# Kernel tuning notes

Measured on AMD Instinct MI355X. Metric: run time of the kernel, lower is better.

The kernel has to match this reference:

```python
import jax, jax.numpy as jnp
import numpy as np

B, T, X = 64, 8192, 32
LARGE_NUMBER = 1.0e6  # padding value for invalid (t' > t) entries in the original O(T^2) formulation


def setup_inputs() -> dict:
    key = jax.random.key(0)
    k1, k2 = jax.random.split(key)
    trace1 = jax.random.normal(k1, (B, T, X), dtype=jnp.float32)  # robustness trace of phi (time-reversed)
    trace2 = jax.random.normal(k2, (B, T, X), dtype=jnp.float32)  # robustness trace of psi (time-reversed)
    return {"trace1": trace1, "trace2": trace2}


def _until_trace(phi, psi):
    # phi, psi: [B, T, X] time-reversed traces (index 0 = final time step).
    # Original math (hard min/max, scale=-1, interval=None):
    #   out[j] = max_{j' <= j} min( psi[j'], min_{k in [j', j]} phi[k] )
    # which collapses exactly to the online recurrence:
    #   out[j] = min( phi[j], max( psi[j], out[j-1] ) ),  out[-1] = -LARGE_NUMBER
    # (min with a constant distributes over max). Single O(T) pass instead of O(T^2).
    phi_t = jnp.moveaxis(phi, 1, 0)  # [T, B, X]
    psi_t = jnp.moveaxis(psi, 1, 0)  # [T, B, X]
    init = jnp.full(phi_t.shape[1:], -LARGE_NUMBER, dtype=phi.dtype)  # [B, X]

    def step(carry, pp):
        p1, p2 = pp
        out = jnp.minimum(p1, jnp.maximum(p2, carry))
        return out, out

    _, outs = jax.lax.scan(step, init, (phi_t, psi_t))  # outs: [T, B, X]
    return jnp.moveaxis(outs, 0, 1)  # [B, T, X]


def reference(trace1, trace2):
    # Subformulas are Identity (pscale=1): robustness traces are the inputs themselves.
    return _until_trace(trace1, trace2)


if __name__ == "__main__":
    out = jax.jit(reference)(**setup_inputs())
    print(out.shape, out.dtype)
```

## Files before the change

kernel.cpp:

```cpp
#include <hip/hip_runtime.h>
#include <math.h>

constexpr int B_  = 64;
constexpr int T_  = 8192;
constexpr int X_  = 32;
constexpr int CH  = 256;
constexpr int TC  = T_ / CH;
constexpr int XG  = X_ / 4;
constexpr int CPL = CH / 64;
constexpr float NEG_LARGE = -1.0e6f;

typedef float vf4 __attribute__((ext_vector_type(4)));


__device__ __forceinline__ float4 clamp4(const float4 L, const float4 H, const float4 c) {
    return make_float4(fminf(H.x, fmaxf(L.x, c.x)),
                       fminf(H.y, fmaxf(L.y, c.y)),
                       fminf(H.z, fmaxf(L.z, c.z)),
                       fminf(H.w, fmaxf(L.w, c.w)));
}

__device__ __forceinline__ void compose_pair(const float4 p, const float4 q,
                                             float4& L, float4& H) {
    float l;
    l = fminf(p.x, q.x); L.x = fminf(p.x, fmaxf(l, L.x)); H.x = fminf(p.x, fmaxf(l, H.x));
    l = fminf(p.y, q.y); L.y = fminf(p.y, fmaxf(l, L.y)); H.y = fminf(p.y, fmaxf(l, H.y));
    l = fminf(p.z, q.z); L.z = fminf(p.z, fmaxf(l, L.z)); H.z = fminf(p.z, fmaxf(l, H.z));
    l = fminf(p.w, q.w); L.w = fminf(p.w, fmaxf(l, L.w)); H.w = fminf(p.w, fmaxf(l, H.w));
}

__device__ __forceinline__ void apply_step(const float4 p, const float4 q, float4& c) {
    c.x = fminf(p.x, fmaxf(q.x, c.x));
    c.y = fminf(p.y, fmaxf(q.y, c.y));
    c.z = fminf(p.z, fmaxf(q.z, c.z));
    c.w = fminf(p.w, fmaxf(q.w, c.w));
}

__device__ __forceinline__ float4 shfl_up4(const float4 v, int d) {
    return make_float4(__shfl_up(v.x, d, 64), __shfl_up(v.y, d, 64),
                       __shfl_up(v.z, d, 64), __shfl_up(v.w, d, 64));
}

__global__ __launch_bounds__(256) void until_pass1(
        const float4* __restrict__ phi, const float4* __restrict__ psi,
        float4* __restrict__ Lw, float4* __restrict__ Hw) {
    const int tid = blockIdx.x * 256 + threadIdx.x;
    const int xg  = tid & (XG - 1);
    const int bj  = tid / XG;
    const int j   = bj & (CH - 1);
    const int b   = bj / CH;
    const size_t base = ((size_t)b * T_ + (size_t)j * TC) * XG + xg;

    float4 L = make_float4(-INFINITY, -INFINITY, -INFINITY, -INFINITY);
    float4 H = make_float4( INFINITY,  INFINITY,  INFINITY,  INFINITY);
    #pragma unroll 4
    for (int t = 0; t < TC; ++t) {
        const float4 p = phi[base + (size_t)t * XG];
        const float4 q = psi[base + (size_t)t * XG];
        compose_pair(p, q, L, H);
    }
    Lw[(size_t)bj * XG + xg] = L;
    Hw[(size_t)bj * XG + xg] = H;
}

__global__ __launch_bounds__(256) void until_pass2(
        const float4* __restrict__ Lw, const float4* __restrict__ Hw,
        float4* __restrict__ Cw) {
    const int tid  = blockIdx.x * 256 + threadIdx.x;
    const int lane = tid & 63;
    const int w    = tid >> 6;
    const int xg   = w & (XG - 1);
    const int b    = w / XG;

    float4 cL[CPL], cH[CPL];
    float4 L = make_float4(-INFINITY, -INFINITY, -INFINITY, -INFINITY);
    float4 H = make_float4( INFINITY,  INFINITY,  INFINITY,  INFINITY);
    #pragma unroll
    for (int k = 0; k < CPL; ++k) {
        const int j = lane * CPL + k;
        const size_t idx = ((size_t)b * CH + j) * XG + xg;
        cL[k] = Lw[idx];
        cH[k] = Hw[idx];
        L = clamp4(cL[k], cH[k], L);
        H = clamp4(cL[k], cH[k], H);
    }

    #pragma unroll
    for (int d = 1; d < 64; d <<= 1) {
        const float4 Lp = shfl_up4(L, d);
        const float4 Hp = shfl_up4(H, d);
        if (lane >= d) {
            const float4 nL = clamp4(L, H, Lp);
            const float4 nH = clamp4(L, H, Hp);
            L = nL; H = nH;
        }
    }

    const float4 Lex = shfl_up4(L, 1);
    const float4 Hex = shfl_up4(H, 1);
    const float4 c0 = make_float4(NEG_LARGE, NEG_LARGE, NEG_LARGE, NEG_LARGE);
    float4 c = (lane == 0) ? c0 : clamp4(Lex, Hex, c0);

    #pragma unroll
    for (int k = 0; k < CPL; ++k) {
        const int j = lane * CPL + k;
        const size_t idx = ((size_t)b * CH + j) * XG + xg;
        Cw[idx] = c;
        c = clamp4(cL[k], cH[k], c);
    }
}

__global__ __launch_bounds__(256) void until_pass3(
        const float4* __restrict__ phi, const float4* __restrict__ psi,
        const float4* __restrict__ Cw, float4* __restrict__ out) {
    const int tid = blockIdx.x * 256 + threadIdx.x;
    const int xg  = tid & (XG - 1);
    const int bj  = tid / XG;
    const int j   = bj & (CH - 1);
    const int b   = bj / CH;
    const size_t base = ((size_t)b * T_ + (size_t)j * TC) * XG + xg;

    float4 c = Cw[(size_t)bj * XG + xg];
    #pragma unroll 4
    for (int t = 0; t < TC; ++t) {
        const float4 p = phi[base + (size_t)t * XG];
        const float4 q = psi[base + (size_t)t * XG];
        apply_step(p, q, c);
        vf4 cv; cv.x = c.x; cv.y = c.y; cv.z = c.z; cv.w = c.w;
        __builtin_nontemporal_store(cv, reinterpret_cast<vf4*>(&out[base + (size_t)t * XG]));
    }
}

extern "C" void kernel_launch(void* const* d_in, const int* in_sizes, int n_in,
                              void* d_out, int out_size, void* d_ws, size_t ws_size,
                              hipStream_t stream) {
    const float4* phi = (const float4*)d_in[0];
    const float4* psi = (const float4*)d_in[1];
    float4* out = (float4*)d_out;

    const size_t nsum = (size_t)B_ * CH * XG;
    float4* Lw = (float4*)d_ws;
    float4* Hw = Lw + nsum;
    float4* Cw = Hw + nsum;

    const int threads_main = B_ * CH * XG;
    until_pass1<<<threads_main / 256, 256, 0, stream>>>(phi, psi, Lw, Hw);
    until_pass2<<<(B_ * XG * 64) / 256, 256, 0, stream>>>(Lw, Hw, Cw);
    until_pass3<<<threads_main / 256, 256, 0, stream>>>(phi, psi, Cw, out);
}
```

Before: 208.3 us.

## Double chunk count, batch loads for memory-level parallelism, reuse workspace in scan

The chunk count CH becomes a template parameter, and the launcher picks 512 chunks when the workspace is large enough, doubling the thread count in passes 1 and 3. Those passes now issue eight phi loads and eight psi loads before computing, which increases outstanding memory requests per thread. Pass 2 no longer holds chunk summaries in registers: it reloads them and writes the carry-in values back over Lw in place, dropping the separate Cw buffer. The trade-offs are a longer in-warp scan (8 chunks per lane) and a redundant reload in pass 2.

```diff
diff --git a/kernel.cpp b/kernel.cpp
--- a/kernel.cpp
+++ b/kernel.cpp
@@ -4,10 +4,7 @@
 constexpr int B_  = 64;
 constexpr int T_  = 8192;
 constexpr int X_  = 32;
-constexpr int CH  = 256;
-constexpr int TC  = T_ / CH;
 constexpr int XG  = X_ / 4;
-constexpr int CPL = CH / 64;
 constexpr float NEG_LARGE = -1.0e6f;
 
 typedef float vf4 __attribute__((ext_vector_type(4)));
@@ -41,9 +38,11 @@
                        __shfl_up(v.z, d, 64), __shfl_up(v.w, d, 64));
 }
 
+template<int CH>
 __global__ __launch_bounds__(256) void until_pass1(
         const float4* __restrict__ phi, const float4* __restrict__ psi,
         float4* __restrict__ Lw, float4* __restrict__ Hw) {
+    constexpr int TC = T_ / CH;
     const int tid = blockIdx.x * 256 + threadIdx.x;
     const int xg  = tid & (XG - 1);
     const int bj  = tid / XG;
@@ -53,36 +52,40 @@
 
     float4 L = make_float4(-INFINITY, -INFINITY, -INFINITY, -INFINITY);
     float4 H = make_float4( INFINITY,  INFINITY,  INFINITY,  INFINITY);
-    #pragma unroll 4
-    for (int t = 0; t < TC; ++t) {
-        const float4 p = phi[base + (size_t)t * XG];
-        const float4 q = psi[base + (size_t)t * XG];
-        compose_pair(p, q, L, H);
+    constexpr int BATCH = 8;
+    for (int t0 = 0; t0 < TC; t0 += BATCH) {
+        float4 p[BATCH], q[BATCH];
+        #pragma unroll
+        for (int k = 0; k < BATCH; ++k) p[k] = phi[base + (size_t)(t0 + k) * XG];
+        #pragma unroll
+        for (int k = 0; k < BATCH; ++k) q[k] = psi[base + (size_t)(t0 + k) * XG];
+        #pragma unroll
+        for (int k = 0; k < BATCH; ++k) compose_pair(p[k], q[k], L, H);
     }
     Lw[(size_t)bj * XG + xg] = L;
     Hw[(size_t)bj * XG + xg] = H;
 }
 
+template<int CH>
 __global__ __launch_bounds__(256) void until_pass2(
-        const float4* __restrict__ Lw, const float4* __restrict__ Hw,
-        float4* __restrict__ Cw) {
+        float4* __restrict__ Lw, const float4* __restrict__ Hw) {
+    constexpr int CPL = CH / 64;
     const int tid  = blockIdx.x * 256 + threadIdx.x;
     const int lane = tid & 63;
     const int w    = tid >> 6;
     const int xg   = w & (XG - 1);
     const int b    = w / XG;
+    const size_t rowbase = (size_t)b * CH * XG + xg;
 
-    float4 cL[CPL], cH[CPL];
     float4 L = make_float4(-INFINITY, -INFINITY, -INFINITY, -INFINITY);
     float4 H = make_float4( INFINITY,  INFINITY,  INFINITY,  INFINITY);
     #pragma unroll
     for (int k = 0; k < CPL; ++k) {
-        const int j = lane * CPL + k;
-        const size_t idx = ((size_t)b * CH + j) * XG + xg;
-        cL[k] = Lw[idx];
-        cH[k] = Hw[idx];
-        L = clamp4(cL[k], cH[k], L);
-        H = clamp4(cL[k], cH[k], H);
+        const size_t idx = rowbase + (size_t)(lane * CPL + k) * XG;
+        const float4 lL = Lw[idx];
+        const float4 lH = Hw[idx];
+        L = clamp4(lL, lH, L);
+        H = clamp4(lL, lH, H);
     }
 
     #pragma unroll
@@ -103,16 +106,19 @@
 
     #pragma unroll
     for (int k = 0; k < CPL; ++k) {
-        const int j = lane * CPL + k;
-        const size_t idx = ((size_t)b * CH + j) * XG + xg;
-        Cw[idx] = c;
-        c = clamp4(cL[k], cH[k], c);
+        const size_t idx = rowbase + (size_t)(lane * CPL + k) * XG;
+        const float4 lL = Lw[idx];
+        const float4 lH = Hw[idx];
+        Lw[idx] = c;
+        c = clamp4(lL, lH, c);
     }
 }
 
+template<int CH>
 __global__ __launch_bounds__(256) void until_pass3(
         const float4* __restrict__ phi, const float4* __restrict__ psi,
         const float4* __restrict__ Cw, float4* __restrict__ out) {
+    constexpr int TC = T_ / CH;
     const int tid = blockIdx.x * 256 + threadIdx.x;
     const int xg  = tid & (XG - 1);
     const int bj  = tid / XG;
@@ -121,14 +127,33 @@
     const size_t base = ((size_t)b * T_ + (size_t)j * TC) * XG + xg;
 
     float4 c = Cw[(size_t)bj * XG + xg];
-    #pragma unroll 4
-    for (int t = 0; t < TC; ++t) {
-        const float4 p = phi[base + (size_t)t * XG];
-        const float4 q = psi[base + (size_t)t * XG];
-        apply_step(p, q, c);
-        vf4 cv; cv.x = c.x; cv.y = c.y; cv.z = c.z; cv.w = c.w;
-        __builtin_nontemporal_store(cv, reinterpret_cast<vf4*>(&out[base + (size_t)t * XG]));
+    constexpr int BATCH = 8;
+    for (int t0 = 0; t0 < TC; t0 += BATCH) {
+        float4 p[BATCH], q[BATCH];
+        #pragma unroll
+        for (int k = 0; k < BATCH; ++k) p[k] = phi[base + (size_t)(t0 + k) * XG];
+        #pragma unroll
+        for (int k = 0; k < BATCH; ++k) q[k] = psi[base + (size_t)(t0 + k) * XG];
+        #pragma unroll
+        for (int k = 0; k < BATCH; ++k) {
+            apply_step(p[k], q[k], c);
+            vf4 cv; cv.x = c.x; cv.y = c.y; cv.z = c.z; cv.w = c.w;
+            __builtin_nontemporal_store(cv,
+                reinterpret_cast<vf4*>(&out[base + (size_t)(t0 + k) * XG]));
+        }
     }
+}
+
+template<int CH>
+static void launch_all(const float4* phi, const float4* psi, float4* out,
+                       void* d_ws, hipStream_t stream) {
+    const size_t nsum = (size_t)B_ * CH * XG;
+    float4* Lw = (float4*)d_ws;
+    float4* Hw = Lw + nsum;
+    const int threads_main = B_ * CH * XG;
+    until_pass1<CH><<<threads_main / 256, 256, 0, stream>>>(phi, psi, Lw, Hw);
+    until_pass2<CH><<<(B_ * XG * 64) / 256, 256, 0, stream>>>(Lw, Hw);
+    until_pass3<CH><<<threads_main / 256, 256, 0, stream>>>(phi, psi, Lw, out);
 }
 
 extern "C" void kernel_launch(void* const* d_in, const int* in_sizes, int n_in,
@@ -138,13 +163,10 @@
     const float4* psi = (const float4*)d_in[1];
     float4* out = (float4*)d_out;
 
-    const size_t nsum = (size_t)B_ * CH * XG;
-    float4* Lw = (float4*)d_ws;
-    float4* Hw = Lw + nsum;
-    float4* Cw = Hw + nsum;
-
-    const int threads_main = B_ * CH * XG;
-    until_pass1<<<threads_main / 256, 256, 0, stream>>>(phi, psi, Lw, Hw);
-    until_pass2<<<(B_ * XG * 64) / 256, 256, 0, stream>>>(Lw, Hw, Cw);
-    until_pass3<<<threads_main / 256, 256, 0, stream>>>(phi, psi, Cw, out);
+    const size_t need512 = 2ull * B_ * 512 * XG * sizeof(float4);
+    if (ws_size >= need512) {
+        launch_all<512>(phi, psi, out, d_ws, stream);
+    } else {
+        launch_all<256>(phi, psi, out, d_ws, stream);
+    }
 }
```

Result: faster. 199.3 us (-4.3%).

## Fuse three-pass until scan into single kernel with decoupled lookback

Applied to the files above, without the earlier changes.

Replaces the three-kernel reduce/scan/apply pipeline with one kernel. Each block loads its 256-step segment into registers, combines clamp operators within the wavefront and across waves in LDS, then publishes a block aggregate and walks back serially over earlier segments' flagged aggregates. Phi and psi are read once instead of twice, and two launches plus the workspace round-trips go away. The flags are never reset between calls, so a later call can read a previous run's aggregates before the current ones are written. It also relies on earlier blocks being scheduled first to avoid spinning forever.

```diff
diff --git a/kernel.cpp b/kernel.cpp
--- a/kernel.cpp
+++ b/kernel.cpp
@@ -1,23 +1,23 @@
 #include <hip/hip_runtime.h>
 #include <math.h>
 
-constexpr int B_  = 64;
-constexpr int T_  = 8192;
-constexpr int X_  = 32;
-constexpr int CH  = 256;
-constexpr int TC  = T_ / CH;
-constexpr int XG  = X_ / 4;
-constexpr int CPL = CH / 64;
+constexpr int B_   = 64;
+constexpr int T_   = 8192;
+constexpr int XG   = 8;
+constexpr int SEGS = 32;
+constexpr int TSEG = T_ / SEGS;
+constexpr int TC   = 8;
 constexpr float NEG_LARGE = -1.0e6f;
+constexpr unsigned AGG_MAGIC = 0x1F2E3D4Cu;
 
 typedef float vf4 __attribute__((ext_vector_type(4)));
 
 
-__device__ __forceinline__ float4 clamp4(const float4 L, const float4 H, const float4 c) {
-    return make_float4(fminf(H.x, fmaxf(L.x, c.x)),
-                       fminf(H.y, fmaxf(L.y, c.y)),
-                       fminf(H.z, fmaxf(L.z, c.z)),
-                       fminf(H.w, fmaxf(L.w, c.w)));
+__device__ __forceinline__ float4 clamp4(const float4 lo, const float4 hi, const float4 c) {
+    return make_float4(fminf(hi.x, fmaxf(lo.x, c.x)),
+                       fminf(hi.y, fmaxf(lo.y, c.y)),
+                       fminf(hi.z, fmaxf(lo.z, c.z)),
+                       fminf(hi.w, fmaxf(lo.w, c.w)));
 }
 
 __device__ __forceinline__ void compose_pair(const float4 p, const float4 q,
@@ -41,52 +41,38 @@
                        __shfl_up(v.z, d, 64), __shfl_up(v.w, d, 64));
 }
 
-__global__ __launch_bounds__(256) void until_pass1(
+__global__ __launch_bounds__(256) void until_fused(
         const float4* __restrict__ phi, const float4* __restrict__ psi,
-        float4* __restrict__ Lw, float4* __restrict__ Hw) {
-    const int tid = blockIdx.x * 256 + threadIdx.x;
-    const int xg  = tid & (XG - 1);
-    const int bj  = tid / XG;
-    const int j   = bj & (CH - 1);
-    const int b   = bj / CH;
-    const size_t base = ((size_t)b * T_ + (size_t)j * TC) * XG + xg;
+        float4* __restrict__ out, float4* __restrict__ agg,
+        unsigned* __restrict__ flags) {
+    const int g    = blockIdx.x;
+    const int b    = g >> 5;
+    const int seg  = g & (SEGS - 1);
+    const int tid  = threadIdx.x;
+    const int w    = tid >> 6;
+    const int lane = tid & 63;
+    const int jl   = lane >> 3;
+    const int xg   = lane & 7;
+    const int cb   = w * 8 + jl;
+    const size_t base = ((size_t)b * T_ + (size_t)seg * TSEG + (size_t)cb * TC) * XG + xg;
+
+    __shared__ float4 swL[4][XG];
+    __shared__ float4 swH[4][XG];
+    __shared__ float4 cLDS[XG];
+
+    float4 p[TC], q[TC];
+    #pragma unroll
+    for (int k = 0; k < TC; ++k) p[k] = phi[base + (size_t)k * XG];
+    #pragma unroll
+    for (int k = 0; k < TC; ++k) q[k] = psi[base + (size_t)k * XG];
 
     float4 L = make_float4(-INFINITY, -INFINITY, -INFINITY, -INFINITY);
     float4 H = make_float4( INFINITY,  INFINITY,  INFINITY,  INFINITY);
-    #pragma unroll 4
-    for (int t = 0; t < TC; ++t) {
-        const float4 p = phi[base + (size_t)t * XG];
-        const float4 q = psi[base + (size_t)t * XG];
-        compose_pair(p, q, L, H);
-    }
-    Lw[(size_t)bj * XG + xg] = L;
-    Hw[(size_t)bj * XG + xg] = H;
-}
-
-__global__ __launch_bounds__(256) void until_pass2(
-        const float4* __restrict__ Lw, const float4* __restrict__ Hw,
-        float4* __restrict__ Cw) {
-    const int tid  = blockIdx.x * 256 + threadIdx.x;
-    const int lane = tid & 63;
-    const int w    = tid >> 6;
-    const int xg   = w & (XG - 1);
-    const int b    = w / XG;
-
-    float4 cL[CPL], cH[CPL];
-    float4 L = make_float4(-INFINITY, -INFINITY, -INFINITY, -INFINITY);
-    float4 H = make_float4( INFINITY,  INFINITY,  INFINITY,  INFINITY);
     #pragma unroll
-    for (int k = 0; k < CPL; ++k) {
-        const int j = lane * CPL + k;
-        const size_t idx = ((size_t)b * CH + j) * XG + xg;
-        cL[k] = Lw[idx];
-        cH[k] = Hw[idx];
-        L = clamp4(cL[k], cH[k], L);
-        H = clamp4(cL[k], cH[k], H);
-    }
+    for (int k = 0; k < TC; ++k) compose_pair(p[k], q[k], L, H);
 
     #pragma unroll
-    for (int d = 1; d < 64; d <<= 1) {
+    for (int d = 8; d < 64; d <<= 1) {
         const float4 Lp = shfl_up4(L, d);
         const float4 Hp = shfl_up4(H, d);
         if (lane >= d) {
@@ -96,38 +82,67 @@
         }
     }
 
-    const float4 Lex = shfl_up4(L, 1);
-    const float4 Hex = shfl_up4(H, 1);
-    const float4 c0 = make_float4(NEG_LARGE, NEG_LARGE, NEG_LARGE, NEG_LARGE);
-    float4 c = (lane == 0) ? c0 : clamp4(Lex, Hex, c0);
+    if (jl == 7) { swL[w][xg] = L; swH[w][xg] = H; }
+    __syncthreads();
+
+    float4 wcL = make_float4(-INFINITY, -INFINITY, -INFINITY, -INFINITY);
+    float4 wcH = make_float4( INFINITY,  INFINITY,  INFINITY,  INFINITY);
+    for (int ww = 0; ww < w; ++ww) {
+        const float4 sL = swL[ww][xg], sH = swH[ww][xg];
+        const float4 nL = clamp4(sL, sH, wcL);
+        const float4 nH = clamp4(sL, sH, wcH);
+        wcL = nL; wcH = nH;
+    }
+
+    if (tid < 8) {
+        float4 BL = make_float4(-INFINITY, -INFINITY, -INFINITY, -INFINITY);
+        float4 BH = make_float4( INFINITY,  INFINITY,  INFINITY,  INFINITY);
+        #pragma unroll
+        for (int ww = 0; ww < 4; ++ww) {
+            const float4 sL = swL[ww][tid], sH = swH[ww][tid];
+            const float4 nL = clamp4(sL, sH, BL);
+            const float4 nH = clamp4(sL, sH, BH);
+            BL = nL; BH = nH;
+        }
+        agg[(size_t)g * 16 + tid * 2 + 0] = BL;
+        agg[(size_t)g * 16 + tid * 2 + 1] = BH;
+        __threadfence();
+        if (tid == 0)
+            __hip_atomic_store(&flags[(size_t)g * 16], AGG_MAGIC,
+                               __ATOMIC_RELEASE, __HIP_MEMORY_SCOPE_AGENT);
+
+        float4 aL = make_float4(-INFINITY, -INFINITY, -INFINITY, -INFINITY);
+        float4 aH = make_float4( INFINITY,  INFINITY,  INFINITY,  INFINITY);
+        for (int k = seg - 1; k >= 0; --k) {
+            const int gk = g - (seg - k);
+            while (__hip_atomic_load(&flags[(size_t)gk * 16],
+                                     __ATOMIC_ACQUIRE, __HIP_MEMORY_SCOPE_AGENT)
+                   != AGG_MAGIC) {
+                __builtin_amdgcn_s_sleep(1);
+            }
+            const float4 fL = agg[(size_t)gk * 16 + tid * 2 + 0];
+            const float4 fH = agg[(size_t)gk * 16 + tid * 2 + 1];
+            const float4 nL = clamp4(aL, aH, fL);
+            const float4 nH = clamp4(aL, aH, fH);
+            aL = nL; aH = nH;
+        }
+        const float4 neg4 = make_float4(NEG_LARGE, NEG_LARGE, NEG_LARGE, NEG_LARGE);
+        cLDS[tid] = clamp4(aL, aH, neg4);
+    }
+    __syncthreads();
+
+    float4 c = cLDS[xg];
+    c = clamp4(wcL, wcH, c);
+    const float4 exL = shfl_up4(L, 8);
+    const float4 exH = shfl_up4(H, 8);
+    if (jl > 0) c = clamp4(exL, exH, c);
 
     #pragma unroll
-    for (int k = 0; k < CPL; ++k) {
-        const int j = lane * CPL + k;
-        const size_t idx = ((size_t)b * CH + j) * XG + xg;
-        Cw[idx] = c;
-        c = clamp4(cL[k], cH[k], c);
-    }
-}
-
-__global__ __launch_bounds__(256) void until_pass3(
-        const float4* __restrict__ phi, const float4* __restrict__ psi,
-        const float4* __restrict__ Cw, float4* __restrict__ out) {
-    const int tid = blockIdx.x * 256 + threadIdx.x;
-    const int xg  = tid & (XG - 1);
-    const int bj  = tid / XG;
-    const int j   = bj & (CH - 1);
-    const int b   = bj / CH;
-    const size_t base = ((size_t)b * T_ + (size_t)j * TC) * XG + xg;
-
-    float4 c = Cw[(size_t)bj * XG + xg];
-    #pragma unroll 4
-    for (int t = 0; t < TC; ++t) {
-        const float4 p = phi[base + (size_t)t * XG];
-        const float4 q = psi[base + (size_t)t * XG];
-        apply_step(p, q, c);
+    for (int k = 0; k < TC; ++k) {
+        apply_step(p[k], q[k], c);
         vf4 cv; cv.x = c.x; cv.y = c.y; cv.z = c.z; cv.w = c.w;
-        __builtin_nontemporal_store(cv, reinterpret_cast<vf4*>(&out[base + (size_t)t * XG]));
+        __builtin_nontemporal_store(cv,
+            reinterpret_cast<vf4*>(&out[base + (size_t)k * XG]));
     }
 }
 
@@ -138,13 +153,8 @@
     const float4* psi = (const float4*)d_in[1];
     float4* out = (float4*)d_out;
 
-    const size_t nsum = (size_t)B_ * CH * XG;
-    float4* Lw = (float4*)d_ws;
-    float4* Hw = Lw + nsum;
-    float4* Cw = Hw + nsum;
+    float4*   agg   = (float4*)d_ws;
+    unsigned* flags = (unsigned*)((char*)d_ws + (size_t)B_ * SEGS * 16 * sizeof(float4));
 
-    const int threads_main = B_ * CH * XG;
-    until_pass1<<<threads_main / 256, 256, 0, stream>>>(phi, psi, Lw, Hw);
-    until_pass2<<<(B_ * XG * 64) / 256, 256, 0, stream>>>(Lw, Hw, Cw);
-    until_pass3<<<threads_main / 256, 256, 0, stream>>>(phi, psi, Cw, out);
+    until_fused<<<B_ * SEGS, 256, 0, stream>>>(phi, psi, out, agg, flags);
 }
```

Result: slower. 563.7 us (+170.6%).
